# Kernel optimization log

Hardware: AMD Instinct MI355X
Metric: run time of the kernel (lower is better)

The kernel has to match this reference:

```python
import jax, jax.numpy as jnp
import numpy as np

C = 64       # class_number (from json groups)
D = 256      # out_dimension = predicted.shape[1]
N = 262144   # batch size


def setup_inputs() -> dict:
    key = jax.random.key(0)
    k1, k2, k3, k4 = jax.random.split(key, 4)
    predicted = jax.random.normal(k1, (N, D), dtype=jnp.float32)
    target = jax.random.randint(k2, (N,), 0, C)
    centroids = jax.random.normal(k3, (C, D), dtype=jnp.float32)
    # accumulated per-class distance sums are nonnegative (sqrt is applied)
    distances = jax.random.uniform(k4, (C, 1), dtype=jnp.float32) * float(N)
    # count = bincount(target) as the torch module accumulates; clamp >= 1
    ones = jnp.ones((N,), jnp.float32)
    count = jnp.maximum(jax.ops.segment_sum(ones, target, num_segments=C), 1.0)[:, None]
    # build_class_weight_matrix: single group containing every label -> all 1.5
    class_weights = jnp.full((C, C), 1.5, dtype=jnp.float32)
    return dict(predicted=predicted, centroids=centroids, distances=distances,
                count=count, class_weights=class_weights, target=target)


def reference(predicted, centroids, distances, count, class_weights, target):
    # === calculate_loss path (epoch % 3 == 2) ===
    C_ = centroids.shape[0]
    sel_counts = count[target]            # [N,1] gather
    sel_centroids = centroids[target]     # [N,D] gather
    pr = predicted / sel_counts           # [N,D]
    cent_new = centroids.at[target].add(pr)                 # scatter-add
    vec = jnp.linalg.norm(sel_centroids - pr, axis=1)       # [N]
    s = distances.at[target].add(vec[:, None])              # scatter-add [C,1]
    s = jnp.sqrt(s) / count                                 # [C,1]
    # cdist(cent_new, cent_new, p=2) via the norm trick
    sq = jnp.sum(cent_new * cent_new, axis=1)               # [C]
    d2 = jnp.maximum(sq[:, None] + sq[None, :] - 2.0 * (cent_new @ cent_new.T), 0.0)
    mask = ~jnp.eye(C_, dtype=bool)
    m = jnp.sqrt(jnp.where(mask, d2, 1.0))                  # safe off-diagonal sqrt
    S = s + s.T                                             # s[i] + s[j], [C,C]
    term = jnp.where(mask, class_weights * S / m, 0.0)
    sum_ = jnp.sum(term)
    loss = sum_ / C_ * (C_ - 1)
    return loss + jnp.sum(jnp.abs(cent_new)) / 1000000.0
```

## Files before the change

### kernel.cpp

```cpp
#include <hip/hip_runtime.h>
#include <math.h>

#define NROWS 262144
#define DIM   256
#define NC    64
#define CD    (NC*DIM)
#define NBLK  512

#define OFF_CENT   0
#define OFF_SF     16384
#define OFF_ABS    16448
#define OFF_PAIR   16512
#define OFF_SPART  16576
#define OFF_SST2   49344
#define OFF_ST2    50368
#define OFF_PART   115904

typedef short  bf16x8 __attribute__((ext_vector_type(8)));
typedef float  f32x16 __attribute__((ext_vector_type(16)));

#define DPP_ADD(v, ctrl) \
    ((v) + __int_as_float(__builtin_amdgcn_update_dpp(0, __float_as_int(v), (ctrl), 0xf, 0xf, true)))

__device__ __forceinline__ float dpp_sum64(float v) {
    v = DPP_ADD(v, 0x111);
    v = DPP_ADD(v, 0x112);
    v = DPP_ADD(v, 0x114);
    v = DPP_ADD(v, 0x118);
    v = DPP_ADD(v, 0x142);
    v = DPP_ADD(v, 0x143);
    return v;
}

__device__ __forceinline__ unsigned int bf16rne2(float lo, float hi) {
    unsigned int ul = __float_as_uint(lo);
    ul = (ul + 0x7FFFu + ((ul >> 16) & 1u)) >> 16;
    unsigned int uh = __float_as_uint(hi);
    uh = (uh + 0x7FFFu + ((uh >> 16) & 1u)) & 0xFFFF0000u;
    return ul | uh;
}

__device__ __forceinline__ void do_mfma_chunk(const unsigned short* pb,
                                              const int* tgts, int rbase,
                                              int lane, int d0,
                                              f32x16& a0r, f32x16& a1r)
{
    const int g8  = (lane >> 5) << 3;
    const int cA  = lane & 31;
    const int cB  = 32 + cA;
    const int col = d0 + cA;
    #pragma unroll
    for (int ks = 0; ks < 4; ++ks) {
        const int rA = rbase + ks * 16 + g8;
        const int t0 = tgts[rA+0], t1 = tgts[rA+1], t2 = tgts[rA+2], t3 = tgts[rA+3];
        const int t4 = tgts[rA+4], t5 = tgts[rA+5], t6 = tgts[rA+6], t7 = tgts[rA+7];
        union { unsigned int u[4]; bf16x8 v; } A0, A1, B;
        A0.u[0] = ((t0==cA)?0x3F80u:0u) | (((t1==cA)?0x3F80u:0u) << 16);
        A0.u[1] = ((t2==cA)?0x3F80u:0u) | (((t3==cA)?0x3F80u:0u) << 16);
        A0.u[2] = ((t4==cA)?0x3F80u:0u) | (((t5==cA)?0x3F80u:0u) << 16);
        A0.u[3] = ((t6==cA)?0x3F80u:0u) | (((t7==cA)?0x3F80u:0u) << 16);
        A1.u[0] = ((t0==cB)?0x3F80u:0u) | (((t1==cB)?0x3F80u:0u) << 16);
        A1.u[1] = ((t2==cB)?0x3F80u:0u) | (((t3==cB)?0x3F80u:0u) << 16);
        A1.u[2] = ((t4==cB)?0x3F80u:0u) | (((t5==cB)?0x3F80u:0u) << 16);
        A1.u[3] = ((t6==cB)?0x3F80u:0u) | (((t7==cB)?0x3F80u:0u) << 16);
        const int kr = ks * 16 + g8;
        #pragma unroll
        for (int p = 0; p < 4; ++p) {
            const unsigned int lo = pb[(kr + 2*p    ) * 256 + col];
            const unsigned int hi = pb[(kr + 2*p + 1) * 256 + col];
            B.u[p] = lo | (hi << 16);
        }
        a0r = __builtin_amdgcn_mfma_f32_32x32x16_bf16(A0.v, B.v, a0r, 0, 0, 0);
        a1r = __builtin_amdgcn_mfma_f32_32x32x16_bf16(A1.v, B.v, a1r, 0, 0, 0);
    }
}

__global__ __launch_bounds__(512, 4)
void k_main(const float* __restrict__ pred, const float* __restrict__ cent,
            const float* __restrict__ count, const int* __restrict__ tgt,
            float* __restrict__ ws)
{
    __shared__ unsigned short pbf[2][64 * 256];
    __shared__ int   tgt_s[512];
    __shared__ float inv_s[64];
    __shared__ float vec_s[512];
    __shared__ float sw_s[8][64];

    const int tid  = threadIdx.x;
    const int w    = tid >> 6;
    const int lane = tid & 63;
    const int base = blockIdx.x * 512;

    tgt_s[tid] = tgt[base + tid];
    if (tid < 64) inv_s[tid] = 1.0f / count[tid];
    __syncthreads();

    const float4* pred4 = (const float4*)pred;
    const float4* cent4 = (const float4*)cent;
    const int d0 = w * 32;

    f32x16 acc0 = {};
    f32x16 acc1 = {};

    float4 p0, p1, p2, p3, p4, p5, p6, p7;

#define LOADCH(cc) {                                                           \
    const size_t gr = (size_t)(base + (cc) * 64) * 64 + lane;                  \
    p0 = pred4[gr + (size_t)( 0 + w) * 64];                                    \
    p1 = pred4[gr + (size_t)( 8 + w) * 64];                                    \
    p2 = pred4[gr + (size_t)(16 + w) * 64];                                    \
    p3 = pred4[gr + (size_t)(24 + w) * 64];                                    \
    p4 = pred4[gr + (size_t)(32 + w) * 64];                                    \
    p5 = pred4[gr + (size_t)(40 + w) * 64];                                    \
    p6 = pred4[gr + (size_t)(48 + w) * 64];                                    \
    p7 = pred4[gr + (size_t)(56 + w) * 64]; }

#define ROW(pp, i, cc, b)                                                      \
    {                                                                          \
        const int rc = 8*(i) + w;                                              \
        const int r  = (cc)*64 + rc;                                           \
        const int c  = tgt_s[r];                                               \
        const float iv = inv_s[c];                                             \
        const float4 ce = cent4[(size_t)c * 64 + lane];                        \
        const float dx = ce.x - pp.x * iv, dy = ce.y - pp.y * iv;              \
        const float dz = ce.z - pp.z * iv, dw = ce.w - pp.w * iv;              \
        float ss = dx*dx + dy*dy + dz*dz + dw*dw;                              \
        ss = dpp_sum64(ss);                                                    \
        if (lane == 63) vec_s[r] = sqrtf(ss);                                  \
        *(uint2*)&pbf[b][rc * 256 + lane * 4] =                                \
            make_uint2(bf16rne2(pp.x, pp.y), bf16rne2(pp.z, pp.w));            \
    }

#define ROWS8(cc, b)                                                           \
    ROW(p0, 0, cc, b) ROW(p1, 1, cc, b) ROW(p2, 2, cc, b) ROW(p3, 3, cc, b)    \
    ROW(p4, 4, cc, b) ROW(p5, 5, cc, b) ROW(p6, 6, cc, b) ROW(p7, 7, cc, b)

    LOADCH(0)
    ROWS8(0, 0)
    __syncthreads();

    #pragma unroll 1
    for (int ch = 0; ch < 7; ++ch) {
        const int cur = ch & 1;
        LOADCH(ch + 1)
        do_mfma_chunk(pbf[cur], tgt_s, ch * 64, lane, d0, acc0, acc1);
        ROWS8(ch + 1, cur ^ 1)
        __syncthreads();
    }
    do_mfma_chunk(pbf[1], tgt_s, 7 * 64, lane, d0, acc0, acc1);

    float* pp = ws + OFF_PART + (size_t)blockIdx.x * CD;
    const int dim = d0 + (lane & 31);
    #pragma unroll
    for (int reg = 0; reg < 16; ++reg) {
        const int crow = (reg & 3) + 8 * (reg >> 2) + 4 * (lane >> 5);
        pp[(     crow) * 256 + dim] = acc0[reg];
        pp[(32 + crow) * 256 + dim] = acc1[reg];
    }

    {
        const float vv = vec_s[w * 64 + lane];
        const int   cc = tgt_s[w * 64 + lane];
        float accs = 0.f;
        for (int k = 0; k < NC; ++k) {
            float sel = (cc == k) ? vv : 0.f;
            sel = dpp_sum64(sel);
            const float tot = __shfl(sel, 63, 64);
            accs += (lane == k) ? tot : 0.f;
        }
        sw_s[w][lane] = accs;
    }
    __syncthreads();
    if (w == 0) {
        float s = 0.f;
        #pragma unroll
        for (int q = 0; q < 8; ++q) s += sw_s[q][lane];
        ws[OFF_SPART + blockIdx.x * 64 + lane] = s;
    }
#undef LOADCH
#undef ROW
#undef ROWS8
}

__global__ __launch_bounds__(256)
void k_red(float* __restrict__ ws)
{
    const int b = blockIdx.x, t = threadIdx.x;
    __shared__ float red[4][64];
    if (b < 1024) {
        const int pg = b >> 8, eg = b & 255;
        const int e  = eg * 64 + (t & 63);
        const int ps = t >> 6;
        const float* pp = ws + OFF_PART + e;
        float s = 0.f;
        const int pstart = pg * 128 + ps * 32;
        #pragma unroll 8
        for (int p = pstart; p < pstart + 32; ++p) s += pp[(size_t)p * CD];
        red[ps][t & 63] = s;
        __syncthreads();
        if (t < 64)
            ws[OFF_ST2 + pg * CD + eg * 64 + t]
                = red[0][t] + red[1][t] + red[2][t] + red[3][t];
    } else {
        const int q = b - 1024;
        const int c = t & 63, pq = t >> 6;
        float s = 0.f;
        #pragma unroll
        for (int i = 0; i < 8; ++i)
            s += ws[OFF_SPART + (q * 32 + pq * 8 + i) * 64 + c];
        red[pq][c] = s;
        __syncthreads();
        if (t < 64)
            ws[OFF_SST2 + q * 64 + t]
                = red[0][t] + red[1][t] + red[2][t] + red[3][t];
    }
}

__global__ __launch_bounds__(256)
void k2_build(const float* __restrict__ cent, const float* __restrict__ count,
              const float* __restrict__ dist, float* __restrict__ ws)
{
    const int c = blockIdx.x, i = threadIdx.x;
    const float inv = 1.0f / count[c];
    const int o = c * 256 + i;
    float tsum = 0.f;
    #pragma unroll
    for (int pg = 0; pg < 4; ++pg) tsum += ws[OFF_ST2 + pg * CD + o];
    const float val = cent[o] + tsum * inv;
    ws[OFF_CENT + o] = val;
    float a = fabsf(val);
    #pragma unroll
    for (int off = 32; off > 0; off >>= 1) a += __shfl_xor(a, off, 64);
    __shared__ float ra[4];
    if ((i & 63) == 0) ra[i >> 6] = a;
    __syncthreads();
    if (i == 0) {
        float sv = 0.f;
        #pragma unroll
        for (int q = 0; q < 16; ++q) sv += ws[OFF_SST2 + q * 64 + c];
        ws[OFF_ABS + c] = ra[0] + ra[1] + ra[2] + ra[3];
        ws[OFF_SF  + c] = sqrtf(dist[c] + sv) / count[c];
    }
}

__global__ __launch_bounds__(256)
void k3_pairs(const float* __restrict__ cw, float* __restrict__ ws)
{
    const int i    = blockIdx.x;
    const int tid  = threadIdx.x;
    const int lane = tid & 63;
    const int w    = tid >> 6;
    const float4* c4 = (const float4*)(ws + OFF_CENT);
    const float*  sf = ws + OFF_SF;

    float4 ci = c4[i * 64 + lane];
    float  si = sf[i];
    float acc = 0.f;
    for (int j = w; j < NC; j += 4) {
        if (j == i) continue;
        float4 cj = c4[j * 64 + lane];
        float dx = ci.x - cj.x, dy = ci.y - cj.y;
        float dz = ci.z - cj.z, dw = ci.w - cj.w;
        float ss = dx*dx + dy*dy + dz*dz + dw*dw;
        #pragma unroll
        for (int o = 32; o > 0; o >>= 1) ss += __shfl_xor(ss, o, 64);
        acc += cw[i * NC + j] * (si + sf[j]) / sqrtf(ss);
    }
    __shared__ float wsum[4];
    if (lane == 0) wsum[w] = acc;
    __syncthreads();
    if (tid == 0) ws[OFF_PAIR + i] = wsum[0] + wsum[1] + wsum[2] + wsum[3];
}

__global__ __launch_bounds__(64)
void k4_final(const float* __restrict__ ws, float* __restrict__ out)
{
    const int t = threadIdx.x;
    float a = ws[OFF_ABS + t];
    float p = ws[OFF_PAIR + t];
    #pragma unroll
    for (int o = 32; o > 0; o >>= 1) {
        a += __shfl_xor(a, o, 64);
        p += __shfl_xor(p, o, 64);
    }
    if (t == 0) out[0] = p / 64.0f * 63.0f + a * 1e-6f;
}

extern "C" void kernel_launch(void* const* d_in, const int* in_sizes, int n_in,
                              void* d_out, int out_size, void* d_ws, size_t ws_size,
                              hipStream_t stream)
{
    const float* pred  = (const float*)d_in[0];
    const float* cent  = (const float*)d_in[1];
    const float* dist  = (const float*)d_in[2];
    const float* count = (const float*)d_in[3];
    const float* cw    = (const float*)d_in[4];
    const int*   tgt   = (const int*)d_in[5];
    float* ws  = (float*)d_ws;
    float* out = (float*)d_out;

    k_main  <<<NBLK, 512, 0, stream>>>(pred, cent, count, tgt, ws);
    k_red   <<<1040, 256, 0, stream>>>(ws);
    k2_build<<<NC,   256, 0, stream>>>(cent, count, dist, ws);
    k3_pairs<<<NC,   256, 0, stream>>>(cw, ws);
    k4_final<<<1,     64, 0, stream>>>(ws, out);
}
```

Measured before the change: 92.82 us.

## Stage centroids as bf16 in LDS and drop double-buffered pipeline

```diff
diff --git a/kernel.cpp b/kernel.cpp
--- a/kernel.cpp
+++ b/kernel.cpp
@@ -39,6 +39,8 @@
     uh = (uh + 0x7FFFu + ((uh >> 16) & 1u)) & 0xFFFF0000u;
     return ul | uh;
 }
+__device__ __forceinline__ float bflo(unsigned int u) { return __uint_as_float(u << 16); }
+__device__ __forceinline__ float bfhi(unsigned int u) { return __uint_as_float(u & 0xFFFF0000u); }
 
 __device__ __forceinline__ void do_mfma_chunk(const unsigned short* pb,
                                               const int* tgts, int rbase,
@@ -80,7 +82,8 @@
             const float* __restrict__ count, const int* __restrict__ tgt,
             float* __restrict__ ws)
 {
-    __shared__ unsigned short pbf[2][64 * 256];
+    __shared__ unsigned short pbf[64 * 256];
+    __shared__ unsigned short cbf[NC * 256];
     __shared__ int   tgt_s[512];
     __shared__ float inv_s[64];
     __shared__ float vec_s[512];
@@ -93,61 +96,60 @@
 
     tgt_s[tid] = tgt[base + tid];
     if (tid < 64) inv_s[tid] = 1.0f / count[tid];
+    {
+        const float2* c2 = (const float2*)cent;
+        unsigned int* cb32 = (unsigned int*)cbf;
+        #pragma unroll
+        for (int i = 0; i < 16; ++i) {
+            const int o = i * 512 + tid;
+            const float2 cf = c2[o];
+            cb32[o] = bf16rne2(cf.x, cf.y);
+        }
+    }
     __syncthreads();
 
     const float4* pred4 = (const float4*)pred;
-    const float4* cent4 = (const float4*)cent;
     const int d0 = w * 32;
 
     f32x16 acc0 = {};
     f32x16 acc1 = {};
 
-    float4 p0, p1, p2, p3, p4, p5, p6, p7;
-
-#define LOADCH(cc) {                                                           \
-    const size_t gr = (size_t)(base + (cc) * 64) * 64 + lane;                  \
-    p0 = pred4[gr + (size_t)( 0 + w) * 64];                                    \
-    p1 = pred4[gr + (size_t)( 8 + w) * 64];                                    \
-    p2 = pred4[gr + (size_t)(16 + w) * 64];                                    \
-    p3 = pred4[gr + (size_t)(24 + w) * 64];                                    \
-    p4 = pred4[gr + (size_t)(32 + w) * 64];                                    \
-    p5 = pred4[gr + (size_t)(40 + w) * 64];                                    \
-    p6 = pred4[gr + (size_t)(48 + w) * 64];                                    \
-    p7 = pred4[gr + (size_t)(56 + w) * 64]; }
-
-#define ROW(pp, i, cc, b)                                                      \
-    {                                                                          \
-        const int rc = 8*(i) + w;                                              \
-        const int r  = (cc)*64 + rc;                                           \
-        const int c  = tgt_s[r];                                               \
-        const float iv = inv_s[c];                                             \
-        const float4 ce = cent4[(size_t)c * 64 + lane];                        \
-        const float dx = ce.x - pp.x * iv, dy = ce.y - pp.y * iv;              \
-        const float dz = ce.z - pp.z * iv, dw = ce.w - pp.w * iv;              \
-        float ss = dx*dx + dy*dy + dz*dz + dw*dw;                              \
-        ss = dpp_sum64(ss);                                                    \
-        if (lane == 63) vec_s[r] = sqrtf(ss);                                  \
-        *(uint2*)&pbf[b][rc * 256 + lane * 4] =                                \
-            make_uint2(bf16rne2(pp.x, pp.y), bf16rne2(pp.z, pp.w));            \
-    }
-
-#define ROWS8(cc, b)                                                           \
-    ROW(p0, 0, cc, b) ROW(p1, 1, cc, b) ROW(p2, 2, cc, b) ROW(p3, 3, cc, b)    \
-    ROW(p4, 4, cc, b) ROW(p5, 5, cc, b) ROW(p6, 6, cc, b) ROW(p7, 7, cc, b)
-
-    LOADCH(0)
-    ROWS8(0, 0)
-    __syncthreads();
-
     #pragma unroll 1
-    for (int ch = 0; ch < 7; ++ch) {
-        const int cur = ch & 1;
-        LOADCH(ch + 1)
-        do_mfma_chunk(pbf[cur], tgt_s, ch * 64, lane, d0, acc0, acc1);
-        ROWS8(ch + 1, cur ^ 1)
+    for (int ch = 0; ch < 8; ++ch) {
+        const size_t gr = (size_t)(base + ch * 64) * 64 + lane;
+        float4 p0 = pred4[gr + (size_t)( 0 + w) * 64];
+        float4 p1 = pred4[gr + (size_t)( 8 + w) * 64];
+        float4 p2 = pred4[gr + (size_t)(16 + w) * 64];
+        float4 p3 = pred4[gr + (size_t)(24 + w) * 64];
+        float4 p4 = pred4[gr + (size_t)(32 + w) * 64];
+        float4 p5 = pred4[gr + (size_t)(40 + w) * 64];
+        float4 p6 = pred4[gr + (size_t)(48 + w) * 64];
+        float4 p7 = pred4[gr + (size_t)(56 + w) * 64];
+
+#define ROW(pp, i)                                                             \
+        {                                                                      \
+            const int rc = 8*(i) + w;                                          \
+            const int r  = ch * 64 + rc;                                       \
+            const int c  = tgt_s[r];                                           \
+            const float iv = inv_s[c];                                         \
+            const uint2 cu = *(const uint2*)&cbf[c * 256 + lane * 4];          \
+            const float dx = bflo(cu.x) - pp.x * iv;                           \
+            const float dy = bfhi(cu.x) - pp.y * iv;                           \
+            const float dz = bflo(cu.y) - pp.z * iv;                           \
+            const float dw = bfhi(cu.y) - pp.w * iv;                           \
+            float ss = dx*dx + dy*dy + dz*dz + dw*dw;                          \
+            ss = dpp_sum64(ss);                                                \
+            if (lane == 63) vec_s[r] = sqrtf(ss);                              \
+            *(uint2*)&pbf[rc * 256 + lane * 4] =                               \
+                make_uint2(bf16rne2(pp.x, pp.y), bf16rne2(pp.z, pp.w));        \
+        }
+        ROW(p0, 0) ROW(p1, 1) ROW(p2, 2) ROW(p3, 3)
+        ROW(p4, 4) ROW(p5, 5) ROW(p6, 6) ROW(p7, 7)
+#undef ROW
         __syncthreads();
-    }
-    do_mfma_chunk(pbf[1], tgt_s, 7 * 64, lane, d0, acc0, acc1);
+        do_mfma_chunk(pbf, tgt_s, ch * 64, lane, d0, acc0, acc1);
+        __syncthreads();
+    }
 
     float* pp = ws + OFF_PART + (size_t)blockIdx.x * CD;
     const int dim = d0 + (lane & 31);
@@ -177,9 +179,6 @@
         for (int q = 0; q < 8; ++q) s += sw_s[q][lane];
         ws[OFF_SPART + blockIdx.x * 64 + lane] = s;
     }
-#undef LOADCH
-#undef ROW
-#undef ROWS8
 }
 
 __global__ __launch_bounds__(256)
```

New measurement: 85.15 us. 8.3% less time.
